# Optimization experiments

Hardware: AMD Instinct MI355X
Metric: run time of the kernel (lower is better)

Reference implementation:

```python
import jax
import jax.numpy as jnp
import numpy as np

EPS = 1e-06


def _topk_mask(scores, k):
    # scores: (T, E); hard top-k mask along last dim
    _, idx = jax.lax.top_k(scores, k)            # (T, k)
    hard = jax.nn.one_hot(idx, scores.shape[-1]).sum(axis=-2)  # (T, E)
    return hard.astype(bool)


def setup_inputs() -> dict:
    key = jax.random.key(0)
    k1, k2, k3 = jax.random.split(key, 3)
    T, D, E = 8192, 4096, 64
    h_td = jax.random.normal(k1, (T, D), dtype=jnp.float32)
    # eqx.nn.Linear weight layout: (out_features, in_features)
    W = jax.random.normal(k2, (E, D), dtype=jnp.float32) * (1.0 / np.sqrt(D))
    bias_e = jax.random.normal(k3, (E,), dtype=jnp.float32)
    return {"h_td": h_td, "W": W, "bias_e": bias_e, "k": 8}


def reference(h_td, W, bias_e, k):
    # Linear(d_model -> E), no bias in proj; external bias_e added after
    logits_te = jnp.einsum("td,ed->te", h_td, W) + bias_e[None, :]  # (T, E)
    # Soft combine weights always from clean logits
    weight_te = jax.nn.softmax(logits_te, axis=-1)
    # Training path: Gumbel noise on the selection scores only
    gkey = jax.random.key(42)
    u = jax.random.uniform(gkey, logits_te.shape, minval=EPS, maxval=1.0 - EPS)
    g = -jnp.log(-jnp.log(u))
    sel_scores = logits_te + g
    mask_te = _topk_mask(sel_scores, k)
    return (mask_te, weight_te, logits_te)
```

## Files before the change

kernel.cpp:

```cpp
#include <hip/hip_runtime.h>
#include <stdint.h>
#include <math.h>

#define T_DIM 8192
#define D_DIM 4096
#define E_DIM 64
#define TE (T_DIM * E_DIM)
#define GAP_MARGIN 2e-3
#define ROWS 16
#define NKSTEP (D_DIM / 32)
#define FIX_WAVES 8
#define FIX_COLS (D_DIM / FIX_WAVES)

typedef __attribute__((ext_vector_type(8))) short short8_t;
typedef __attribute__((ext_vector_type(4))) float f32x4;

__device__ __align__(16) short Whi_g[E_DIM * D_DIM];
__device__ __align__(16) short Wlo_g[E_DIM * D_DIM];

__device__ __forceinline__ void threefry2x32_k42(uint32_t x0, uint32_t x1,
                                                 uint32_t& o0, uint32_t& o1) {
  const uint32_t ks0 = 0u, ks1 = 42u;
  const uint32_t ks2 = 0x1BD11BDAu ^ ks0 ^ ks1;
  x0 += ks0; x1 += ks1;
#define TF_RND(r) { x0 += x1; x1 = (x1 << (r)) | (x1 >> (32 - (r))); x1 ^= x0; }
  TF_RND(13) TF_RND(15) TF_RND(26) TF_RND(6)   x0 += ks1; x1 += ks2 + 1u;
  TF_RND(17) TF_RND(29) TF_RND(16) TF_RND(24)  x0 += ks2; x1 += ks0 + 2u;
  TF_RND(13) TF_RND(15) TF_RND(26) TF_RND(6)   x0 += ks0; x1 += ks1 + 3u;
  TF_RND(17) TF_RND(29) TF_RND(16) TF_RND(24)  x0 += ks1; x1 += ks2 + 4u;
  TF_RND(13) TF_RND(15) TF_RND(26) TF_RND(6)   x0 += ks2; x1 += ks0 + 5u;
#undef TF_RND
  o0 = x0; o1 = x1;
}

__device__ __forceinline__ uint32_t jax_random_bits32(uint32_t j) {
  uint32_t o0, o1;
  threefry2x32_k42(0u, j, o0, o1);
  return o0 ^ o1;
}

__device__ __forceinline__ void finalize_row_f64(double logit, int e, int t,
                                                 float& mask_out, float& weight_out,
                                                 double& gap_out) {
  double m = logit;
#pragma unroll
  for (int off = 1; off < 64; off <<= 1) {
    const double om = __shfl_xor(m, off, 64);
    m = (om > m) ? om : m;
  }
  const double pe = exp(logit - m);
  double s = pe;
#pragma unroll
  for (int off = 1; off < 64; off <<= 1) s += __shfl_xor(s, off, 64);
  weight_out = (float)(pe / s);

  const int idx = t * 64 + e;
  const uint32_t bits = jax_random_bits32((uint32_t)idx);
  const float f01 = __uint_as_float((bits >> 9) | 0x3f800000u) - 1.0f;
  const float minv = 1e-6f;
  const float maxv = 0.999999f;
  float u = __fadd_rn(__fmul_rn(f01, maxv - minv), minv);
  u = fmaxf(minv, u);
  const double g = -log(-log((double)u));
  const double sel = logit + g;

  float mask = 0.0f;
  double cur = sel;
  double v8 = 0.0, v9 = 0.0;
  for (int it = 0; it < 9; ++it) {
    double v = cur;
    int vi = e;
#pragma unroll
    for (int off = 1; off < 64; off <<= 1) {
      const double ov = __shfl_xor(v, off, 64);
      const int    oi = __shfl_xor(vi, off, 64);
      if (ov > v || (ov == v && oi < vi)) { v = ov; vi = oi; }
    }
    if (it < 8) {
      if (vi == e) { mask = 1.0f; cur = -__builtin_inf(); }
      if (it == 7) v8 = v;
    } else {
      v9 = v;
    }
  }
  mask_out = mask;
  gap_out = v8 - v9;
}

__device__ __forceinline__ uint16_t f2bf(float f) {
  const uint32_t x = __float_as_uint(f);
  return (uint16_t)((x + 0x7FFFu + ((x >> 16) & 1u)) >> 16);
}

__device__ __forceinline__ void split8(const float4 a, const float4 b,
                                       short8_t& hi, short8_t& lo) {
  const float f[8] = {a.x, a.y, a.z, a.w, b.x, b.y, b.z, b.w};
#pragma unroll
  for (int j = 0; j < 8; ++j) {
    const uint16_t hb = f2bf(f[j]);
    const float fh = __uint_as_float((uint32_t)hb << 16);
    const uint16_t lb = f2bf(f[j] - fh);
    hi[j] = (short)hb;
    lo[j] = (short)lb;
  }
}

__global__ __launch_bounds__(256)
void w_split_kernel(const float* __restrict__ W) {
  const int g = blockIdx.x * 256 + threadIdx.x;
#pragma unroll
  for (int r = 0; r < 2; ++r) {
    const int u = g * 2 + r;
    const int e = u >> 9;
    const int k0 = (u & 511) * 8;
    const float* wp = W + (size_t)e * D_DIM + k0;
    const float4 a = *reinterpret_cast<const float4*>(wp);
    const float4 b = *reinterpret_cast<const float4*>(wp + 4);
    short8_t hi, lo;
    split8(a, b, hi, lo);
    const int ks = k0 >> 5, q = (k0 >> 3) & 3;
    const int subE = e >> 4, ee = e & 15;
    const int idx = ks * 2048 + subE * 512 + q * 128 + ee * 8;
    *reinterpret_cast<short8_t*>(Whi_g + idx) = hi;
    *reinterpret_cast<short8_t*>(Wlo_g + idx) = lo;
  }
}

__global__ __launch_bounds__(256)
void router_mfma_kernel(const float* __restrict__ h,
                        const float* __restrict__ bias,
                        float* __restrict__ out,
                        unsigned char* __restrict__ flags) {
  __shared__ float logits_lds[ROWS * 65];

  const int tid  = threadIdx.x;
  const int wave = tid >> 6;
  const int lane = tid & 63;
  const int row0 = blockIdx.x * ROWS;

  const int a_row  = lane & 15;
  const int a_koct = lane >> 4;
  const float* aptr = h + (size_t)(row0 + a_row) * D_DIM + a_koct * 8;

  const int b_off = wave * 512 + (lane >> 4) * 128 + (lane & 15) * 8;
  const short* bh_base = Whi_g + b_off;
  const short* bl_base = Wlo_g + b_off;

  f32x4 acc = {0.0f, 0.0f, 0.0f, 0.0f};

#pragma unroll 4
  for (int ks = 0; ks < NKSTEP; ++ks) {
    const float4 a0 = *reinterpret_cast<const float4*>(aptr + ks * 32);
    const float4 a1 = *reinterpret_cast<const float4*>(aptr + ks * 32 + 4);
    const short8_t bh = *reinterpret_cast<const short8_t*>(bh_base + (size_t)ks * 2048);
    const short8_t bl = *reinterpret_cast<const short8_t*>(bl_base + (size_t)ks * 2048);
    short8_t ah, al;
    split8(a0, a1, ah, al);
    acc = __builtin_amdgcn_mfma_f32_16x16x32_bf16(al, bh, acc, 0, 0, 0);
    acc = __builtin_amdgcn_mfma_f32_16x16x32_bf16(ah, bl, acc, 0, 0, 0);
    acc = __builtin_amdgcn_mfma_f32_16x16x32_bf16(ah, bh, acc, 0, 0, 0);
  }

  {
    const int q   = lane >> 4;
    const int col = wave * 16 + (lane & 15);
#pragma unroll
    for (int reg = 0; reg < 4; ++reg) {
      const int m = q * 4 + reg;
      logits_lds[m * 65 + col] = acc[reg];
    }
  }
  __syncthreads();

  const int e = lane;
  const double be = (double)bias[e];
  for (int rr = 0; rr < 4; ++rr) {
    const int rloc = wave * 4 + rr;
    const int t = row0 + rloc;
    const double logit = (double)logits_lds[rloc * 65 + e] + be;

    float mask, weight;
    double gap;
    finalize_row_f64(logit, e, t, mask, weight, gap);

    const int idx = t * 64 + e;
    out[idx]          = mask;
    out[TE + idx]     = weight;
    out[2 * TE + idx] = (float)logit;
    if (e == 0) flags[t] = (gap < GAP_MARGIN) ? 1 : 0;
  }
}

__global__ __launch_bounds__(512)
void router_fixup_kernel(const float* __restrict__ h,
                         const float* __restrict__ W,
                         const float* __restrict__ bias,
                         const unsigned char* __restrict__ flags,
                         float* __restrict__ out) {
  const int t = blockIdx.x;
  if (flags[t] == 0) return;

  __shared__ float  h_lds[D_DIM];
  __shared__ double red[FIX_WAVES][64];

  const int tid  = threadIdx.x;
  const int wv   = tid >> 6;
  const int lane = tid & 63;

  {
    const float4* hrow4 = reinterpret_cast<const float4*>(h + (size_t)t * D_DIM);
    float4* hl4 = reinterpret_cast<float4*>(h_lds);
    hl4[tid]       = hrow4[tid];
    hl4[tid + 512] = hrow4[tid + 512];
  }
  __syncthreads();

  const int e = lane;
  const float* wrow = W + (size_t)e * D_DIM + wv * FIX_COLS;
  const float* hseg = h_lds + wv * FIX_COLS;

  double acc0 = 0.0, acc1 = 0.0, acc2 = 0.0, acc3 = 0.0;
#pragma unroll 8
  for (int c = 0; c < FIX_COLS; c += 16) {
    const float4 w0 = *reinterpret_cast<const float4*>(wrow + c);
    const float4 w1 = *reinterpret_cast<const float4*>(wrow + c + 4);
    const float4 w2 = *reinterpret_cast<const float4*>(wrow + c + 8);
    const float4 w3 = *reinterpret_cast<const float4*>(wrow + c + 12);
    acc0 = fma((double)w0.x, (double)hseg[c + 0], acc0);
    acc0 = fma((double)w0.y, (double)hseg[c + 1], acc0);
    acc0 = fma((double)w0.z, (double)hseg[c + 2], acc0);
    acc0 = fma((double)w0.w, (double)hseg[c + 3], acc0);
    acc1 = fma((double)w1.x, (double)hseg[c + 4], acc1);
    acc1 = fma((double)w1.y, (double)hseg[c + 5], acc1);
    acc1 = fma((double)w1.z, (double)hseg[c + 6], acc1);
    acc1 = fma((double)w1.w, (double)hseg[c + 7], acc1);
    acc2 = fma((double)w2.x, (double)hseg[c + 8], acc2);
    acc2 = fma((double)w2.y, (double)hseg[c + 9], acc2);
    acc2 = fma((double)w2.z, (double)hseg[c + 10], acc2);
    acc2 = fma((double)w2.w, (double)hseg[c + 11], acc2);
    acc3 = fma((double)w3.x, (double)hseg[c + 12], acc3);
    acc3 = fma((double)w3.y, (double)hseg[c + 13], acc3);
    acc3 = fma((double)w3.z, (double)hseg[c + 14], acc3);
    acc3 = fma((double)w3.w, (double)hseg[c + 15], acc3);
  }
  red[wv][e] = (acc0 + acc1) + (acc2 + acc3);
  __syncthreads();

  if (wv == 0) {
    double s = red[0][e];
#pragma unroll
    for (int i = 1; i < FIX_WAVES; ++i) s += red[i][e];
    const double logit = s + (double)bias[e];

    float mask, weight;
    double gap;
    finalize_row_f64(logit, e, t, mask, weight, gap);

    const int idx = t * 64 + e;
    out[idx]          = mask;
    out[TE + idx]     = weight;
    out[2 * TE + idx] = (float)logit;
  }
}

extern "C" void kernel_launch(void* const* d_in, const int* in_sizes, int n_in,
                              void* d_out, int out_size, void* d_ws, size_t ws_size,
                              hipStream_t stream) {
  const float* h    = (const float*)d_in[0];
  const float* W    = (const float*)d_in[1];
  const float* bias = (const float*)d_in[2];
  float* out = (float*)d_out;
  unsigned char* flags = (unsigned char*)d_ws;

  w_split_kernel<<<64, 256, 0, stream>>>(W);
  router_mfma_kernel<<<T_DIM / ROWS, 256, 0, stream>>>(h, bias, out, flags);
  router_fixup_kernel<<<T_DIM, 512, 0, stream>>>(h, W, bias, flags, out);
}
```

Measured before the change: 335.5 us.

## Stage split A tiles in swizzled LDS with register prefetch, shared across waves

Before, each of the 4 waves loaded the same 16 rows of h from global memory and did its own bf16 hi/lo split, so every A element was loaded and converted four times. Now each thread loads a slice of the 16x256 chunk, splits it once, and writes it into double-buffered, XOR-swizzled LDS that all waves read from. Global loads for chunk c+2 are issued into registers before the MFMA work on chunk c, so load latency overlaps compute. The cost is a __syncthreads per chunk, extra LDS traffic and more registers.

```diff
diff --git a/kernel.cpp b/kernel.cpp
--- a/kernel.cpp
+++ b/kernel.cpp
@@ -8,7 +8,8 @@
 #define TE (T_DIM * E_DIM)
 #define GAP_MARGIN 2e-3
 #define ROWS 16
-#define NKSTEP (D_DIM / 32)
+#define BK 256
+#define NCHUNK (D_DIM / BK)
 #define FIX_WAVES 8
 #define FIX_COLS (D_DIM / FIX_WAVES)
 
@@ -131,6 +132,8 @@
                         const float* __restrict__ bias,
                         float* __restrict__ out,
                         unsigned char* __restrict__ flags) {
+  __shared__ __align__(16) short Ahi[2][ROWS * BK];
+  __shared__ __align__(16) short Alo[2][ROWS * BK];
   __shared__ float logits_lds[ROWS * 65];
 
   const int tid  = threadIdx.x;
@@ -138,28 +141,67 @@
   const int lane = tid & 63;
   const int row0 = blockIdx.x * ROWS;
 
-  const int a_row  = lane & 15;
-  const int a_koct = lane >> 4;
-  const float* aptr = h + (size_t)(row0 + a_row) * D_DIM + a_koct * 8;
+  const int r  = tid >> 4;
+  const int k0 = (tid & 15) * 16;
+  const int sA  = k0 >> 5;
+  const int qA  = (k0 >> 3) & 3;
+  const int u0A = sA * 64 + qA * 16 + r;
+  const int u0B = u0A + 16;
+  const int uA  = u0A ^ ((u0A >> 4) & 7);
+  const int uB  = u0B ^ ((u0B >> 4) & 7);
+  const float* hst = h + (size_t)(row0 + r) * D_DIM + k0;
 
   const int b_off = wave * 512 + (lane >> 4) * 128 + (lane & 15) * 8;
-  const short* bh_base = Whi_g + b_off;
-  const short* bl_base = Wlo_g + b_off;
 
   f32x4 acc = {0.0f, 0.0f, 0.0f, 0.0f};
 
-#pragma unroll 4
-  for (int ks = 0; ks < NKSTEP; ++ks) {
-    const float4 a0 = *reinterpret_cast<const float4*>(aptr + ks * 32);
-    const float4 a1 = *reinterpret_cast<const float4*>(aptr + ks * 32 + 4);
-    const short8_t bh = *reinterpret_cast<const short8_t*>(bh_base + (size_t)ks * 2048);
-    const short8_t bl = *reinterpret_cast<const short8_t*>(bl_base + (size_t)ks * 2048);
-    short8_t ah, al;
-    split8(a0, a1, ah, al);
-    acc = __builtin_amdgcn_mfma_f32_16x16x32_bf16(al, bh, acc, 0, 0, 0);
-    acc = __builtin_amdgcn_mfma_f32_16x16x32_bf16(ah, bl, acc, 0, 0, 0);
-    acc = __builtin_amdgcn_mfma_f32_16x16x32_bf16(ah, bh, acc, 0, 0, 0);
-  }
+  float4 Ra0, Ra1, Ra2, Ra3, Rb0, Rb1, Rb2, Rb3;
+  Ra0 = *reinterpret_cast<const float4*>(hst + 0);
+  Ra1 = *reinterpret_cast<const float4*>(hst + 4);
+  Ra2 = *reinterpret_cast<const float4*>(hst + 8);
+  Ra3 = *reinterpret_cast<const float4*>(hst + 12);
+  Rb0 = *reinterpret_cast<const float4*>(hst + BK + 0);
+  Rb1 = *reinterpret_cast<const float4*>(hst + BK + 4);
+  Rb2 = *reinterpret_cast<const float4*>(hst + BK + 8);
+  Rb3 = *reinterpret_cast<const float4*>(hst + BK + 12);
+
+#define CHUNK_STEP(R0, R1, R2, R3, BUF, CC)                                    \
+  {                                                                            \
+    short8_t hi_, lo_;                                                         \
+    split8(R0, R1, hi_, lo_);                                                  \
+    *reinterpret_cast<short8_t*>(&Ahi[BUF][uA * 8]) = hi_;                     \
+    *reinterpret_cast<short8_t*>(&Alo[BUF][uA * 8]) = lo_;                     \
+    split8(R2, R3, hi_, lo_);                                                  \
+    *reinterpret_cast<short8_t*>(&Ahi[BUF][uB * 8]) = hi_;                     \
+    *reinterpret_cast<short8_t*>(&Alo[BUF][uB * 8]) = lo_;                     \
+    __syncthreads();                                                           \
+    if ((CC) + 2 < NCHUNK) {                                                   \
+      const float* p_ = hst + ((CC) + 2) * BK;                                 \
+      R0 = *reinterpret_cast<const float4*>(p_ + 0);                           \
+      R1 = *reinterpret_cast<const float4*>(p_ + 4);                           \
+      R2 = *reinterpret_cast<const float4*>(p_ + 8);                           \
+      R3 = *reinterpret_cast<const float4*>(p_ + 12);                          \
+    }                                                                          \
+    _Pragma("unroll")                                                          \
+    for (int s_ = 0; s_ < BK / 32; ++s_) {                                     \
+      const int ur0_ = s_ * 64 + lane;                                         \
+      const int ur_  = ur0_ ^ ((ur0_ >> 4) & 7);                               \
+      const short8_t ah_ = *reinterpret_cast<const short8_t*>(&Ahi[BUF][ur_ * 8]); \
+      const short8_t al_ = *reinterpret_cast<const short8_t*>(&Alo[BUF][ur_ * 8]); \
+      const size_t bo_ = (size_t)((CC) * (BK / 32) + s_) * 2048 + b_off;       \
+      const short8_t bh_ = *reinterpret_cast<const short8_t*>(Whi_g + bo_);    \
+      const short8_t bl_ = *reinterpret_cast<const short8_t*>(Wlo_g + bo_);    \
+      acc = __builtin_amdgcn_mfma_f32_16x16x32_bf16(al_, bh_, acc, 0, 0, 0);   \
+      acc = __builtin_amdgcn_mfma_f32_16x16x32_bf16(ah_, bl_, acc, 0, 0, 0);   \
+      acc = __builtin_amdgcn_mfma_f32_16x16x32_bf16(ah_, bh_, acc, 0, 0, 0);   \
+    }                                                                          \
+  }
+
+  for (int c = 0; c < NCHUNK; c += 2) {
+    CHUNK_STEP(Ra0, Ra1, Ra2, Ra3, 0, c)
+    CHUNK_STEP(Rb0, Rb1, Rb2, Rb3, 1, c + 1)
+  }
+#undef CHUNK_STEP
 
   {
     const int q   = lane >> 4;
```

Result: no change. 330.6 us (-1.5%).
